# Optimization experiments

Hardware: AMD Instinct MI355X
Metric: run time of the kernel (lower is better)

The kernel has to match this reference:

```python
import jax, jax.numpy as jnp
import numpy as np

H = 64
VOCAB = 64
THRESH_SCALE = 0.4
LN_EPS = 1e-5
NORM_EPS = 1e-12


def setup_inputs() -> dict:
    key = jax.random.key(0)
    ks = jax.random.split(key, 16)
    B, L = 64, 1024
    s = 1.0 / np.sqrt(H)
    inp = {
        "seq": jax.random.randint(ks[0], (B, L), 0, VOCAB),
        "embed_W": jax.random.normal(ks[1], (VOCAB, H), jnp.float32),
        "ff_W1": jax.random.normal(ks[2], (H, 2 * H), jnp.float32) * s,
        "ff_b1": jnp.zeros((2 * H,), jnp.float32),
        "ff_W2": jax.random.normal(ks[3], (2 * H, H), jnp.float32) * s,
        "ff_b2": jnp.zeros((H,), jnp.float32),
        "ln_g": jnp.ones((H,), jnp.float32),
        "ln_b": jnp.zeros((H,), jnp.float32),
        "kp_W": jax.random.normal(ks[4], (H, H), jnp.float32) * s,
        "vp_W": jax.random.normal(ks[5], (H, H), jnp.float32) * s,
        "qp_W": jax.random.normal(ks[6], (H, H), jnp.float32) * s,
        "rp_W": jax.random.normal(ks[7], (H, H), jnp.float32) * s,
        "rp_b": jnp.zeros((H,), jnp.float32),
        "out_W": jax.random.normal(ks[8], (H, VOCAB), jnp.float32) * s,
        "out_b": jnp.zeros((VOCAB,), jnp.float32),
    }
    return inp


def _forward(seq, embed_W, ff_W1, ff_b1, ff_W2, ff_b2, ln_g, ln_b,
             kp_W, vp_W, qp_W, rp_W, rp_b, out_W, out_b):
    h = embed_W[seq]                                    # [B, L, H]
    ff = jnp.maximum(h @ ff_W1 + ff_b1, 0.0) @ ff_W2 + ff_b2
    x = h + ff
    mu = x.mean(-1, keepdims=True)
    var = ((x - mu) ** 2).mean(-1, keepdims=True)       # biased var (torch LayerNorm)
    hn = (x - mu) / jnp.sqrt(var + LN_EPS) * ln_g + ln_b
    B, L, _ = hn.shape

    # Precompute all per-step keys/values, then scan the fast-weight update.
    k_all = hn[:, :-1] @ kp_W                           # [B, L-1, H]
    v_all = hn[:, :-1] @ vp_W                           # [B, L-1, H]
    kn_all = k_all / jnp.maximum(
        jnp.linalg.norm(k_all, axis=-1, keepdims=True), NORM_EPS)

    def step(M, kv):
        kn, v = kv                                      # each [B, H]
        vp = jnp.einsum('bij,bj->bi', M, kn)            # read M along k
        err = jnp.linalg.norm(v - vp, axis=-1)          # [B]
        gate = jnp.where(err > THRESH_SCALE * jnp.linalg.norm(v, axis=-1),
                         1.0, 0.0)                      # hard energy gate
        M = M + gate[:, None, None] * jnp.einsum('bi,bj->bij', v - vp, kn)
        return M, None

    M0 = jnp.zeros((B, H, H), dtype=hn.dtype)
    M, _ = jax.lax.scan(step, M0,
                        (kn_all.transpose(1, 0, 2), v_all.transpose(1, 0, 2)))

    q = hn[:, -1] @ qp_W                                # [B, H]
    r = jnp.einsum('bij,bj->bi', M, q) @ rp_W + rp_b
    return r @ out_W + out_b                            # [B, VOCAB]


def reference(seq, embed_W, ff_W1, ff_b1, ff_W2, ff_b2, ln_g, ln_b,
              kp_W, vp_W, qp_W, rp_W, rp_b, out_W, out_b):
    return _forward(seq, embed_W, ff_W1, ff_b1, ff_W2, ff_b2, ln_g, ln_b,
                    kp_W, vp_W, qp_W, rp_W, rp_b, out_W, out_b)
```

## Files before the change

kernel.cpp:

```cpp
#include <hip/hip_runtime.h>
#include <hip/hip_bf16.h>
#include <math.h>

#define BB 64
#define LL 1024
#define HH 64

typedef float v4f __attribute__((ext_vector_type(4)));
#define F4 __builtin_elementwise_fma

__global__ __launch_bounds__(256, 1)
void token_kernel(const int* __restrict__ seq,
                  const float* __restrict__ embed_W,
                  const float* __restrict__ ff_W1, const float* __restrict__ ff_b1,
                  const float* __restrict__ ff_W2, const float* __restrict__ ff_b2,
                  const float* __restrict__ ln_g, const float* __restrict__ ln_b,
                  const float* __restrict__ kp_W, const float* __restrict__ vp_W,
                  const float* __restrict__ qp_W,
                  float* __restrict__ knv, float* __restrict__ vthr,
                  float* __restrict__ qbuf)
{
    __shared__ __align__(16) float h_s[32][64];
    __shared__ __align__(16) float t1_s[32][128];
    __shared__ __align__(16) float hn_s[32][64];

    const int tid  = threadIdx.x;
    const int tok0 = blockIdx.x * 32;

#pragma unroll
    for (int k = 0; k < 8; ++k) {
        int e   = k * 256 + tid;
        int tok = e >> 6, i = e & 63;
        int s   = seq[tok0 + tok];
        h_s[tok][i] = embed_W[s * 64 + i];
    }
    __syncthreads();

    {
        const int j = tid & 127;
        const int g = tid >> 7;
        float w1c[64];
#pragma unroll
        for (int ii = 0; ii < 64; ++ii) w1c[ii] = ff_W1[ii * 128 + j];
        const float b1j = ff_b1[j];
#pragma unroll
        for (int tk = 0; tk < 16; ++tk) {
            const int tok = g * 16 + tk;
            const float4* h4 = (const float4*)h_s[tok];
            float a0 = b1j, a1 = 0.f, a2 = 0.f, a3 = 0.f;
#pragma unroll
            for (int w = 0; w < 16; ++w) {
                float4 hv = h4[w];
                a0 = fmaf(hv.x, w1c[4*w+0], a0);
                a1 = fmaf(hv.y, w1c[4*w+1], a1);
                a2 = fmaf(hv.z, w1c[4*w+2], a2);
                a3 = fmaf(hv.w, w1c[4*w+3], a3);
            }
            t1_s[tok][j] = fmaxf((a0 + a1) + (a2 + a3), 0.f);
        }
    }
    __syncthreads();

    {
        const int i  = tid & 63;
        const int w4 = tid >> 6;
        const float b2i = ff_b2[i];
        const float gi  = ln_g[i];
        const float bi  = ln_b[i];
        float accf[8];
#pragma unroll
        for (int tk = 0; tk < 8; ++tk) accf[tk] = b2i;
#pragma unroll
        for (int h = 0; h < 2; ++h) {
            float w2c[64];
#pragma unroll
            for (int jj = 0; jj < 64; ++jj) w2c[jj] = ff_W2[(h*64 + jj) * 64 + i];
#pragma unroll
            for (int tk = 0; tk < 8; ++tk) {
                const int tok = w4 * 8 + tk;
                const float4* t4 = (const float4*)&t1_s[tok][h*64];
                float a0 = 0.f, a1 = 0.f, a2 = 0.f, a3 = 0.f;
#pragma unroll
                for (int w = 0; w < 16; ++w) {
                    float4 tv = t4[w];
                    a0 = fmaf(tv.x, w2c[4*w+0], a0);
                    a1 = fmaf(tv.y, w2c[4*w+1], a1);
                    a2 = fmaf(tv.z, w2c[4*w+2], a2);
                    a3 = fmaf(tv.w, w2c[4*w+3], a3);
                }
                accf[tk] += (a0 + a1) + (a2 + a3);
            }
        }
#pragma unroll
        for (int tk = 0; tk < 8; ++tk) {
            const int tok = w4 * 8 + tk;
            float x = h_s[tok][i] + accf[tk];
            float s = x;
#pragma unroll
            for (int m = 32; m > 0; m >>= 1) s += __shfl_xor(s, m);
            float mu = s * (1.f / 64.f);
            float d  = x - mu;
            float s2 = d * d;
#pragma unroll
            for (int m = 32; m > 0; m >>= 1) s2 += __shfl_xor(s2, m);
            float var = s2 * (1.f / 64.f);
            hn_s[tok][i] = d / sqrtf(var + 1e-5f) * gi + bi;
        }
    }
    __syncthreads();

    {
        const int i  = tid & 63;
        const int w4 = tid >> 6;
        float kc[64], vc[64];
#pragma unroll
        for (int ii = 0; ii < 64; ++ii) {
            kc[ii] = kp_W[ii * 64 + i];
            vc[ii] = vp_W[ii * 64 + i];
        }
#pragma unroll
        for (int tk = 0; tk < 8; ++tk) {
            const int tok = w4 * 8 + tk;
            const int tg  = tok0 + tok;
            const int b   = tg >> 10;
            const int t   = tg & 1023;
            const float4* hn4 = (const float4*)hn_s[tok];
            if (t < 1023) {
                float ka0=0.f,ka1=0.f,ka2=0.f,ka3=0.f;
                float va0=0.f,va1=0.f,va2=0.f,va3=0.f;
#pragma unroll
                for (int w = 0; w < 16; ++w) {
                    float4 hv = hn4[w];
                    ka0 = fmaf(hv.x, kc[4*w+0], ka0);
                    ka1 = fmaf(hv.y, kc[4*w+1], ka1);
                    ka2 = fmaf(hv.z, kc[4*w+2], ka2);
                    ka3 = fmaf(hv.w, kc[4*w+3], ka3);
                    va0 = fmaf(hv.x, vc[4*w+0], va0);
                    va1 = fmaf(hv.y, vc[4*w+1], va1);
                    va2 = fmaf(hv.z, vc[4*w+2], va2);
                    va3 = fmaf(hv.w, vc[4*w+3], va3);
                }
                float ka = (ka0 + ka1) + (ka2 + ka3);
                float va = (va0 + va1) + (va2 + va3);
                float kn2 = ka * ka, vn2 = va * va;
#pragma unroll
                for (int m = 32; m > 0; m >>= 1) {
                    kn2 += __shfl_xor(kn2, m);
                    vn2 += __shfl_xor(vn2, m);
                }
                float knorm = fmaxf(sqrtf(kn2), 1e-12f);
                size_t row = ((size_t)b * 1024 + t) * 128;
                knv[row + i]      = ka / knorm;
                knv[row + 64 + i] = va;
                if (i == 0) vthr[b * 1024 + t] = 0.16f * vn2;
            } else {
                float qa0=0.f,qa1=0.f,qa2=0.f,qa3=0.f;
#pragma unroll
                for (int w = 0; w < 16; ++w) {
                    float4 hv = hn4[w];
                    qa0 = fmaf(hv.x, qp_W[(4*w+0)*64 + i], qa0);
                    qa1 = fmaf(hv.y, qp_W[(4*w+1)*64 + i], qa1);
                    qa2 = fmaf(hv.z, qp_W[(4*w+2)*64 + i], qa2);
                    qa3 = fmaf(hv.w, qp_W[(4*w+3)*64 + i], qa3);
                }
                qbuf[b * 64 + i] = (qa0 + qa1) + (qa2 + qa3);
            }
        }
    }
}


template<int CTRL>
__device__ __forceinline__ float dppadd(float x) {
    int y = __builtin_amdgcn_update_dpp(0, __float_as_int(x), CTRL, 0xF, 0xF, true);
    return x + __int_as_float(y);
}

__device__ __forceinline__ float bcast63(float x) {
    return __int_as_float(__builtin_amdgcn_readlane(__float_as_int(x), 63));
}

__device__ __forceinline__ float wave_sum64(float x) {
    x = dppadd<0x111>(x); x = dppadd<0x112>(x);
    x = dppadd<0x114>(x); x = dppadd<0x118>(x);
    x = dppadd<0x142>(x); x = dppadd<0x143>(x);
    return bcast63(x);
}

__device__ __forceinline__ void wsum4(float& a, float& b, float& c, float& d) {
    a = dppadd<0x111>(a); b = dppadd<0x111>(b); c = dppadd<0x111>(c); d = dppadd<0x111>(d);
    a = dppadd<0x112>(a); b = dppadd<0x112>(b); c = dppadd<0x112>(c); d = dppadd<0x112>(d);
    a = dppadd<0x114>(a); b = dppadd<0x114>(b); c = dppadd<0x114>(c); d = dppadd<0x114>(d);
    a = dppadd<0x118>(a); b = dppadd<0x118>(b); c = dppadd<0x118>(c); d = dppadd<0x118>(d);
    a = dppadd<0x142>(a); b = dppadd<0x142>(b); c = dppadd<0x142>(c); d = dppadd<0x142>(d);
    a = dppadd<0x143>(a); b = dppadd<0x143>(b); c = dppadd<0x143>(c); d = dppadd<0x143>(d);
    a = bcast63(a); b = bcast63(b); c = bcast63(c); d = bcast63(d);
}

#define LOADK8(P, ROW) do { \
    const float* rA_ = (ROW) + (wid << 3); \
    const float* rB_ = rA_ + 4; \
    P##A0 = *(const v4f*)(rA_ +  0); P##A1 = *(const v4f*)(rA_ + 16); \
    P##A2 = *(const v4f*)(rA_ + 32); P##A3 = *(const v4f*)(rA_ + 48); \
    P##B0 = *(const v4f*)(rB_ +  0); P##B1 = *(const v4f*)(rB_ + 16); \
    P##B2 = *(const v4f*)(rB_ + 32); P##B3 = *(const v4f*)(rB_ + 48); \
} while (0)

#define UPD8(P, G) do { \
    v4f gv_ = {G, G, G, G}; \
    mA0 = F4(gv_, P##A0, mA0); mA1 = F4(gv_, P##A1, mA1); \
    mA2 = F4(gv_, P##A2, mA2); mA3 = F4(gv_, P##A3, mA3); \
    mB0 = F4(gv_, P##B0, mB0); mB1 = F4(gv_, P##B1, mB1); \
    mB2 = F4(gv_, P##B2, mB2); mB3 = F4(gv_, P##B3, mB3); \
} while (0)

#define CHUNK2(UP, UQ, XR, XS, ROW2, ROW3, TH2P, TH3P, PAR) do { \
    UPD8(UP, gdp); \
    UPD8(UQ, gdq); \
    v4f qa_ = F4(mA0, XR##A0, F4(mA1, XR##A1, F4(mA2, XR##A2, mA3 * XR##A3))); \
    v4f qb_ = F4(mB0, XR##B0, F4(mB1, XR##B1, F4(mB2, XR##B2, mB3 * XR##B3))); \
    v4f q0_ = qa_ + qb_; \
    float own0_ = (q0_.x + q0_.y) + (q0_.z + q0_.w); \
    v4f ra_ = F4(mA0, XS##A0, F4(mA1, XS##A1, F4(mA2, XS##A2, mA3 * XS##A3))); \
    v4f rb_ = F4(mB0, XS##B0, F4(mB1, XS##B1, F4(mB2, XS##B2, mB3 * XS##B3))); \
    v4f r0_ = ra_ + rb_; \
    float own1_ = (r0_.x + r0_.y) + (r0_.z + r0_.w); \
    ((float2*)pex[PAR][wid])[lane] = make_float2(own0_, own1_); \
    asm volatile("s_waitcnt lgkmcnt(0)\n\ts_barrier" ::: "memory"); \
    float2 oth_ = ((const float2*)pex[PAR][1 - wid])[lane]; \
    float knl2_ = (ROW2)[lane]; \
    float knl3_ = (ROW3)[lane]; \
    float vv2_  = (ROW2)[64 + lane]; \
    float vv3_  = (ROW3)[64 + lane]; \
    float th2_  = *(TH2P); \
    float th3_  = *(TH3P); \
    LOADK8(UP, ROW2); \
    LOADK8(UQ, ROW3); \
    float base0_ = own0_ + oth_.x; \
    float base1_ = own1_ + oth_.y; \
    float d00_ = vv0 - base0_; \
    float d01_ = vv1 - base1_; \
    float x0_ = d00_ * d00_, x1_ = d00_ * d01_; \
    float x2_ = d01_ * d01_, x3_ = knl2_ * knl3_; \
    wsum4(x0_, x1_, x2_, x3_); \
    bool g0_ = x0_ > th0; \
    float corr_ = fmaf(2.f * c3, x1_, -(c3 * c3) * x0_); \
    float e1_ = g0_ ? (x2_ - corr_) : x2_; \
    bool g1_ = e1_ > th1; \
    float gd0_ = g0_ ? d00_ : 0.f; \
    float d1_  = fmaf(-c3, gd0_, d01_); \
    gdp = gd0_; \
    gdq = g1_ ? d1_ : 0.f; \
    vv0 = vv2_; vv1 = vv3_; th0 = th2_; th1 = th3_; c3 = x3_; \
} while (0)

#define BUF8(CB, NB, TP) \
    CHUNK2(U,V,S,T,(CB)+2*128, (CB)+3*128, (TP)+2, (TP)+3, 0); \
    CHUNK2(S,T,U,V,(CB)+4*128, (CB)+5*128, (TP)+4, (TP)+5, 1); \
    CHUNK2(U,V,S,T,(CB)+6*128, (CB)+7*128, (TP)+6, (TP)+7, 0); \
    CHUNK2(S,T,U,V,(CB)+8*128, (CB)+9*128, (TP)+8, (TP)+9, 1); \
    CHUNK2(U,V,S,T,(CB)+10*128,(CB)+11*128,(TP)+10,(TP)+11,0); \
    CHUNK2(S,T,U,V,(CB)+12*128,(CB)+13*128,(TP)+12,(TP)+13,1); \
    CHUNK2(U,V,S,T,(CB)+14*128,(CB)+15*128,(TP)+14,(TP)+15,0); \
    CHUNK2(S,T,U,V,(NB)+0*128, (NB)+1*128, (TP)+16,(TP)+17,1);

__device__ __forceinline__ void gl2lds_1k(const float* g, float* l, int lane) {
    __builtin_amdgcn_global_load_lds(
        (const __attribute__((address_space(1))) void*)(g + lane * 4),
        (__attribute__((address_space(3))) void*)l, 16, 0, 0);
}

__device__ __forceinline__ void prefetch_half(const float* g, float* l,
                                              int lane, int wid) {
#pragma unroll
    for (int j = 0; j < 4; ++j)
        gl2lds_1k(g + wid * 1024 + j * 256, l + wid * 1024 + j * 256, lane);
}

__global__ __launch_bounds__(128, 1)
void scan_kernel(const float* __restrict__ knv,
                 const float* __restrict__ vthr,
                 const float* __restrict__ qbuf,
                 const float* __restrict__ rp_W, const float* __restrict__ rp_b,
                 const float* __restrict__ out_W, const float* __restrict__ out_b,
                 float* __restrict__ out)
{
    const int b    = blockIdx.x;
    const int tid  = threadIdx.x;
    const int lane = tid & 63;
    const int wid  = tid >> 6;
    const float* knvb = knv  + (size_t)b * 1024 * 128;
    const float* thrb = vthr + (size_t)b * 1024;

    __shared__ __align__(16) float thr_s[1040];
    __shared__ __align__(16) float buf[3 * 2048];
    __shared__ __align__(16) float pex[2][2][128];
    __shared__ float sh[64];

    v4f mA0={0,0,0,0},mA1={0,0,0,0},mA2={0,0,0,0},mA3={0,0,0,0};
    v4f mB0={0,0,0,0},mB1={0,0,0,0},mB2={0,0,0,0},mB3={0,0,0,0};
    v4f SA0,SA1,SA2,SA3,SB0,SB1,SB2,SB3;
    v4f TA0,TA1,TA2,TA3,TB0,TB1,TB2,TB3;
    v4f UA0,UA1,UA2,UA3,UB0,UB1,UB2,UB3;
    v4f VA0,VA1,VA2,VA3,VB0,VB1,VB2,VB3;

    if (wid == 0) {
#pragma unroll
        for (int w = 0; w < 4; ++w) gl2lds_1k(thrb + w * 256, thr_s + w * 256, lane);
    }
    prefetch_half(knvb,        buf,        lane, wid);
    prefetch_half(knvb + 2048, buf + 2048, lane, wid);
    prefetch_half(knvb + 4096, buf + 4096, lane, wid);

    asm volatile("s_waitcnt vmcnt(4) lgkmcnt(0)\n\ts_barrier" ::: "memory");

    LOADK8(S, buf);
    LOADK8(T, buf + 128);
    {
        v4f z_ = {0.f, 0.f, 0.f, 0.f};
        UA0=z_;UA1=z_;UA2=z_;UA3=z_;UB0=z_;UB1=z_;UB2=z_;UB3=z_;
        VA0=z_;VA1=z_;VA2=z_;VA3=z_;VB0=z_;VB1=z_;VB2=z_;VB3=z_;
    }
    float vv0 = buf[64 + lane];
    float vv1 = buf[192 + lane];
    float th0 = thr_s[0];
    float th1 = thr_s[1];
    float c3  = wave_sum64(buf[lane] * buf[128 + lane]);
    float gdp = 0.f, gdq = 0.f;

#pragma unroll 1
    for (int c = 0; c < 62; ++c) {
        asm volatile("s_waitcnt vmcnt(4)" ::: "memory");
        const float* cb = buf + (c % 3) * 2048;
        const float* nb = buf + ((c + 1) % 3) * 2048;
        const float* tp = thr_s + c * 16;
        BUF8(cb, nb, tp)
        if (c <= 60)
            prefetch_half(knvb + (size_t)(c + 3) * 2048,
                          buf + (c % 3) * 2048, lane, wid);
    }
    asm volatile("s_waitcnt vmcnt(0)" ::: "memory");
    asm volatile("s_barrier" ::: "memory");
    {
        const float* cb = buf + 2 * 2048;
        const float* nb = buf;
        const float* tp = thr_s + 62 * 16;
        BUF8(cb, nb, tp)
    }
    {
        const float* cb = buf;
        const float* nb = buf + 2048;
        const float* tp = thr_s + 63 * 16;
        BUF8(cb, nb, tp)
    }
    UPD8(U, gdp);

    {
        const v4f* qq = (const v4f*)(qbuf + b * 64);
        const int w2 = 2 * wid;
        v4f aqA = F4(mA0, qq[w2+0], F4(mA1, qq[w2+4],
                  F4(mA2, qq[w2+8],  mA3 * qq[w2+12])));
        v4f aqB = F4(mB0, qq[w2+1], F4(mB1, qq[w2+5],
                  F4(mB2, qq[w2+9],  mB3 * qq[w2+13])));
        v4f aq = aqA + aqB;
        float vq_own = (aq.x + aq.y) + (aq.z + aq.w);
        ((float*)pex)[wid * 64 + lane] = vq_own;
        asm volatile("s_waitcnt lgkmcnt(0)\n\ts_barrier" ::: "memory");
        float vq = vq_own + ((float*)pex)[(1 - wid) * 64 + lane];

        if (wid == 0) {
            sh[lane] = vq;
            asm volatile("s_waitcnt lgkmcnt(0)" ::: "memory");
            float r = rp_b[lane];
#pragma unroll
            for (int ii = 0; ii < 64; ++ii) r = fmaf(sh[ii], rp_W[ii * 64 + lane], r);
            asm volatile("s_waitcnt lgkmcnt(0)" ::: "memory");
            sh[lane] = r;
            asm volatile("s_waitcnt lgkmcnt(0)" ::: "memory");
            float o = out_b[lane];
#pragma unroll
            for (int ii = 0; ii < 64; ++ii) o = fmaf(sh[ii], out_W[ii * 64 + lane], o);
            out[b * 64 + lane] = o;
        }
    }
}

extern "C" void kernel_launch(void* const* d_in, const int* in_sizes, int n_in,
                              void* d_out, int out_size, void* d_ws, size_t ws_size,
                              hipStream_t stream)
{
    const int*   seq   = (const int*)  d_in[0];
    const float* embed = (const float*)d_in[1];
    const float* ffW1  = (const float*)d_in[2];
    const float* ffb1  = (const float*)d_in[3];
    const float* ffW2  = (const float*)d_in[4];
    const float* ffb2  = (const float*)d_in[5];
    const float* lng   = (const float*)d_in[6];
    const float* lnb   = (const float*)d_in[7];
    const float* kpW   = (const float*)d_in[8];
    const float* vpW   = (const float*)d_in[9];
    const float* qpW   = (const float*)d_in[10];
    const float* rpW   = (const float*)d_in[11];
    const float* rpb   = (const float*)d_in[12];
    const float* outW  = (const float*)d_in[13];
    const float* outb  = (const float*)d_in[14];
    float* out = (float*)d_out;

    float* knv  = (float*)d_ws;
    float* vthr = knv  + (size_t)64 * 1024 * 128;
    float* qbuf = vthr + (size_t)64 * 1024;

    token_kernel<<<2048, 256, 0, stream>>>(seq, embed, ffW1, ffb1, ffW2, ffb2,
                                           lng, lnb, kpW, vpW, qpW,
                                           knv, vthr, qbuf);
    scan_kernel<<<64, 128, 0, stream>>>(knv, vthr, qbuf,
                                        rpW, rpb, outW, outb, out);
}
```

Measured before the change: 368.6 us.

## Software-pipeline scan step so cross-wave exchange overlaps next step's matvec

Restructures the sequential fast-weight scan so that each step reads the partner wave's partial result written one step earlier, uses a lagged M·k computed before the previous rank-1 updates, and corrects it algebraically with kn dot products (cg0..cg3). This moves the LDS exchange and barrier off the critical dependency chain and batches eight wave reductions together. The prefetch ring grows from three to four buffers so the previous chunk's rows stay resident. It adds extra dot-product reductions and epilogue logic, and its correctness depends on careful buffer indexing.

```diff
diff --git a/kernel.cpp b/kernel.cpp
--- a/kernel.cpp
+++ b/kernel.cpp
@@ -187,14 +187,14 @@
     return bcast63(x);
 }
 
-__device__ __forceinline__ void wsum4(float& a, float& b, float& c, float& d) {
-    a = dppadd<0x111>(a); b = dppadd<0x111>(b); c = dppadd<0x111>(c); d = dppadd<0x111>(d);
-    a = dppadd<0x112>(a); b = dppadd<0x112>(b); c = dppadd<0x112>(c); d = dppadd<0x112>(d);
-    a = dppadd<0x114>(a); b = dppadd<0x114>(b); c = dppadd<0x114>(c); d = dppadd<0x114>(d);
-    a = dppadd<0x118>(a); b = dppadd<0x118>(b); c = dppadd<0x118>(c); d = dppadd<0x118>(d);
-    a = dppadd<0x142>(a); b = dppadd<0x142>(b); c = dppadd<0x142>(c); d = dppadd<0x142>(d);
-    a = dppadd<0x143>(a); b = dppadd<0x143>(b); c = dppadd<0x143>(c); d = dppadd<0x143>(d);
-    a = bcast63(a); b = bcast63(b); c = bcast63(c); d = bcast63(d);
+__device__ __forceinline__ void wsum8(float& a, float& b, float& c, float& d,
+                                      float& e, float& f, float& g, float& h) {
+#define LVL(C) a=dppadd<C>(a); b=dppadd<C>(b); c=dppadd<C>(c); d=dppadd<C>(d); \
+               e=dppadd<C>(e); f=dppadd<C>(f); g=dppadd<C>(g); h=dppadd<C>(h);
+    LVL(0x111) LVL(0x112) LVL(0x114) LVL(0x118) LVL(0x142) LVL(0x143)
+#undef LVL
+    a=bcast63(a); b=bcast63(b); c=bcast63(c); d=bcast63(d);
+    e=bcast63(e); f=bcast63(f); g=bcast63(g); h=bcast63(h);
 }
 
 #define LOADK8(P, ROW) do { \
@@ -214,55 +214,62 @@
     mB2 = F4(gv_, P##B2, mB2); mB3 = F4(gv_, P##B3, mB3); \
 } while (0)
 
-#define CHUNK2(UP, UQ, XR, XS, ROW2, ROW3, TH2P, TH3P, PAR) do { \
-    UPD8(UP, gdp); \
-    UPD8(UQ, gdq); \
-    v4f qa_ = F4(mA0, XR##A0, F4(mA1, XR##A1, F4(mA2, XR##A2, mA3 * XR##A3))); \
-    v4f qb_ = F4(mB0, XR##B0, F4(mB1, XR##B1, F4(mB2, XR##B2, mB3 * XR##B3))); \
+#define BODY(U0R, U1R, X0R, X1R, PK0, PK1, T0P, T1P, PAR) do { \
+    float2 oth_ = ((const float2*)pex[PAR][1 - wid])[lane]; \
+    UPD8(U, gdp); \
+    UPD8(V, gdq); \
+    LOADK8(U, U0R); \
+    LOADK8(V, U1R); \
+    float knl2_ = (PK0)[lane]; \
+    float knl3_ = (PK1)[lane]; \
+    float vv2_  = (PK0)[64 + lane]; \
+    float vv3_  = (PK1)[64 + lane]; \
+    float th2_  = *(T0P); \
+    float th3_  = *(T1P); \
+    v4f qa_ = F4(mA0, SA0, F4(mA1, SA1, F4(mA2, SA2, mA3 * SA3))); \
+    v4f qb_ = F4(mB0, SB0, F4(mB1, SB1, F4(mB2, SB2, mB3 * SB3))); \
     v4f q0_ = qa_ + qb_; \
-    float own0_ = (q0_.x + q0_.y) + (q0_.z + q0_.w); \
-    v4f ra_ = F4(mA0, XS##A0, F4(mA1, XS##A1, F4(mA2, XS##A2, mA3 * XS##A3))); \
-    v4f rb_ = F4(mB0, XS##B0, F4(mB1, XS##B1, F4(mB2, XS##B2, mB3 * XS##B3))); \
+    float own0n_ = (q0_.x + q0_.y) + (q0_.z + q0_.w); \
+    v4f ra_ = F4(mA0, TA0, F4(mA1, TA1, F4(mA2, TA2, mA3 * TA3))); \
+    v4f rb_ = F4(mB0, TB0, F4(mB1, TB1, F4(mB2, TB2, mB3 * TB3))); \
     v4f r0_ = ra_ + rb_; \
-    float own1_ = (r0_.x + r0_.y) + (r0_.z + r0_.w); \
-    ((float2*)pex[PAR][wid])[lane] = make_float2(own0_, own1_); \
+    float own1n_ = (r0_.x + r0_.y) + (r0_.z + r0_.w); \
+    ((float2*)pex[(PAR) ^ 1][wid])[lane] = make_float2(own0n_, own1n_); \
+    LOADK8(S, X0R); \
+    LOADK8(T, X1R); \
+    float base_a_ = pown0 + oth_.x; \
+    float base_b_ = pown1 + oth_.y; \
+    float vp_a_ = fmaf(cg0, gdp, fmaf(cg1, gdq, base_a_)); \
+    float vp_b_ = fmaf(cg2, gdp, fmaf(cg3, gdq, base_b_)); \
+    float da_ = vv_a - vp_a_; \
+    float db_ = vv_b - vp_b_; \
+    float x0_ = da_ * da_, x1_ = da_ * db_, x2_ = db_ * db_; \
+    float y0_ = knl0 * knl2_, y1_ = knl1 * knl2_; \
+    float y2_ = knl0 * knl3_, y3_ = knl1 * knl3_, y4_ = knl2_ * knl3_; \
+    wsum8(x0_, x1_, x2_, y0_, y1_, y2_, y3_, y4_); \
+    bool ga_ = x0_ > th_a; \
+    float corr_ = fmaf(2.f * cab, x1_, -(cab * cab) * x0_); \
+    float eb_ = ga_ ? (x2_ - corr_) : x2_; \
+    bool gb_ = eb_ > th_b; \
+    float gda_ = ga_ ? da_ : 0.f; \
+    float gdb_ = gb_ ? fmaf(-cab, gda_, db_) : 0.f; \
+    gdp = gda_; gdq = gdb_; \
+    cg0 = y0_; cg1 = y1_; cg2 = y2_; cg3 = y3_; cab = y4_; \
+    knl0 = knl2_; knl1 = knl3_; \
+    vv_a = vv2_; vv_b = vv3_; th_a = th2_; th_b = th3_; \
+    pown0 = own0n_; pown1 = own1n_; \
     asm volatile("s_waitcnt lgkmcnt(0)\n\ts_barrier" ::: "memory"); \
-    float2 oth_ = ((const float2*)pex[PAR][1 - wid])[lane]; \
-    float knl2_ = (ROW2)[lane]; \
-    float knl3_ = (ROW3)[lane]; \
-    float vv2_  = (ROW2)[64 + lane]; \
-    float vv3_  = (ROW3)[64 + lane]; \
-    float th2_  = *(TH2P); \
-    float th3_  = *(TH3P); \
-    LOADK8(UP, ROW2); \
-    LOADK8(UQ, ROW3); \
-    float base0_ = own0_ + oth_.x; \
-    float base1_ = own1_ + oth_.y; \
-    float d00_ = vv0 - base0_; \
-    float d01_ = vv1 - base1_; \
-    float x0_ = d00_ * d00_, x1_ = d00_ * d01_; \
-    float x2_ = d01_ * d01_, x3_ = knl2_ * knl3_; \
-    wsum4(x0_, x1_, x2_, x3_); \
-    bool g0_ = x0_ > th0; \
-    float corr_ = fmaf(2.f * c3, x1_, -(c3 * c3) * x0_); \
-    float e1_ = g0_ ? (x2_ - corr_) : x2_; \
-    bool g1_ = e1_ > th1; \
-    float gd0_ = g0_ ? d00_ : 0.f; \
-    float d1_  = fmaf(-c3, gd0_, d01_); \
-    gdp = gd0_; \
-    gdq = g1_ ? d1_ : 0.f; \
-    vv0 = vv2_; vv1 = vv3_; th0 = th2_; th1 = th3_; c3 = x3_; \
 } while (0)
 
-#define BUF8(CB, NB, TP) \
-    CHUNK2(U,V,S,T,(CB)+2*128, (CB)+3*128, (TP)+2, (TP)+3, 0); \
-    CHUNK2(S,T,U,V,(CB)+4*128, (CB)+5*128, (TP)+4, (TP)+5, 1); \
-    CHUNK2(U,V,S,T,(CB)+6*128, (CB)+7*128, (TP)+6, (TP)+7, 0); \
-    CHUNK2(S,T,U,V,(CB)+8*128, (CB)+9*128, (TP)+8, (TP)+9, 1); \
-    CHUNK2(U,V,S,T,(CB)+10*128,(CB)+11*128,(TP)+10,(TP)+11,0); \
-    CHUNK2(S,T,U,V,(CB)+12*128,(CB)+13*128,(TP)+12,(TP)+13,1); \
-    CHUNK2(U,V,S,T,(CB)+14*128,(CB)+15*128,(TP)+14,(TP)+15,0); \
-    CHUNK2(S,T,U,V,(NB)+0*128, (NB)+1*128, (TP)+16,(TP)+17,1);
+#define BUF8_L(PB, CB, NB, TP) \
+    BODY((PB)+14*128,(PB)+15*128,(CB)+2*128,(CB)+3*128,(CB)+0*128,(CB)+1*128,(TP)+0,(TP)+1,0); \
+    BODY((CB)+0*128,(CB)+1*128,(CB)+4*128,(CB)+5*128,(CB)+2*128,(CB)+3*128,(TP)+2,(TP)+3,1); \
+    BODY((CB)+2*128,(CB)+3*128,(CB)+6*128,(CB)+7*128,(CB)+4*128,(CB)+5*128,(TP)+4,(TP)+5,0); \
+    BODY((CB)+4*128,(CB)+5*128,(CB)+8*128,(CB)+9*128,(CB)+6*128,(CB)+7*128,(TP)+6,(TP)+7,1); \
+    BODY((CB)+6*128,(CB)+7*128,(CB)+10*128,(CB)+11*128,(CB)+8*128,(CB)+9*128,(TP)+8,(TP)+9,0); \
+    BODY((CB)+8*128,(CB)+9*128,(CB)+12*128,(CB)+13*128,(CB)+10*128,(CB)+11*128,(TP)+10,(TP)+11,1); \
+    BODY((CB)+10*128,(CB)+11*128,(CB)+14*128,(CB)+15*128,(CB)+12*128,(CB)+13*128,(TP)+12,(TP)+13,0); \
+    BODY((CB)+12*128,(CB)+13*128,(NB)+0*128,(NB)+1*128,(CB)+14*128,(CB)+15*128,(TP)+14,(TP)+15,1);
 
 __device__ __forceinline__ void gl2lds_1k(const float* g, float* l, int lane) {
     __builtin_amdgcn_global_load_lds(
@@ -293,7 +300,7 @@
     const float* thrb = vthr + (size_t)b * 1024;
 
     __shared__ __align__(16) float thr_s[1040];
-    __shared__ __align__(16) float buf[3 * 2048];
+    __shared__ __align__(16) float buf[4 * 2048];
     __shared__ __align__(16) float pex[2][2][128];
     __shared__ float sh[64];
 
@@ -312,48 +319,65 @@
     prefetch_half(knvb + 2048, buf + 2048, lane, wid);
     prefetch_half(knvb + 4096, buf + 4096, lane, wid);
 
+    {
+        float4 z4 = make_float4(0.f, 0.f, 0.f, 0.f);
+        ((float4*)pex)[tid] = z4;
+    }
+
     asm volatile("s_waitcnt vmcnt(4) lgkmcnt(0)\n\ts_barrier" ::: "memory");
 
     LOADK8(S, buf);
     LOADK8(T, buf + 128);
-    {
-        v4f z_ = {0.f, 0.f, 0.f, 0.f};
-        UA0=z_;UA1=z_;UA2=z_;UA3=z_;UB0=z_;UB1=z_;UB2=z_;UB3=z_;
-        VA0=z_;VA1=z_;VA2=z_;VA3=z_;VB0=z_;VB1=z_;VB2=z_;VB3=z_;
-    }
-    float vv0 = buf[64 + lane];
-    float vv1 = buf[192 + lane];
-    float th0 = thr_s[0];
-    float th1 = thr_s[1];
-    float c3  = wave_sum64(buf[lane] * buf[128 + lane]);
+    LOADK8(U, buf);
+    LOADK8(V, buf);
     float gdp = 0.f, gdq = 0.f;
+    float cg0 = 0.f, cg1 = 0.f, cg2 = 0.f, cg3 = 0.f, cab = 0.f;
+    float knl0 = 0.f, knl1 = 0.f;
+    float vv_a = 0.f, vv_b = 0.f;
+    float th_a = 1e30f, th_b = 1e30f;
+    float pown0 = 0.f, pown1 = 0.f;
 
 #pragma unroll 1
     for (int c = 0; c < 62; ++c) {
         asm volatile("s_waitcnt vmcnt(4)" ::: "memory");
-        const float* cb = buf + (c % 3) * 2048;
-        const float* nb = buf + ((c + 1) % 3) * 2048;
+        const float* cb = buf + (c & 3) * 2048;
+        const float* nb = buf + ((c + 1) & 3) * 2048;
+        const float* pb = (c == 0) ? cb : buf + ((c - 1) & 3) * 2048;
         const float* tp = thr_s + c * 16;
-        BUF8(cb, nb, tp)
+        BUF8_L(pb, cb, nb, tp)
         if (c <= 60)
             prefetch_half(knvb + (size_t)(c + 3) * 2048,
-                          buf + (c % 3) * 2048, lane, wid);
+                          buf + ((c + 3) & 3) * 2048, lane, wid);
     }
     asm volatile("s_waitcnt vmcnt(0)" ::: "memory");
     asm volatile("s_barrier" ::: "memory");
     {
+        const float* pb = buf + 1 * 2048;
         const float* cb = buf + 2 * 2048;
+        const float* nb = buf + 3 * 2048;
+        const float* tp = thr_s + 62 * 16;
+        BUF8_L(pb, cb, nb, tp)
+    }
+    {
+        const float* pb = buf + 2 * 2048;
+        const float* cb = buf + 3 * 2048;
         const float* nb = buf;
-        const float* tp = thr_s + 62 * 16;
-        BUF8(cb, nb, tp)
-    }
-    {
-        const float* cb = buf;
-        const float* nb = buf + 2048;
         const float* tp = thr_s + 63 * 16;
-        BUF8(cb, nb, tp)
-    }
-    UPD8(U, gdp);
+        BUF8_L(pb, cb, nb, tp)
+    }
+
+    {
+        float2 oth_ = ((const float2*)pex[0][1 - wid])[lane];
+        UPD8(U, gdp);
+        UPD8(V, gdq);
+        float base_a_ = pown0 + oth_.x;
+        float vp_a_ = fmaf(cg0, gdp, fmaf(cg1, gdq, base_a_));
+        float da_ = vv_a - vp_a_;
+        float e_ = wave_sum64(da_ * da_);
+        float gda_ = (e_ > th_a) ? da_ : 0.f;
+        LOADK8(S, buf + 3 * 2048 + 14 * 128);
+        UPD8(S, gda_);
+    }
 
     {
         const v4f* qq = (const v4f*)(qbuf + b * 64);
```

New measurement: 427.9 us. +16.1%, slower.

## Split scan kernel fast-weight columns across four waves instead of two

Applied to the files above, without the earlier changes.

The sequential scan kernel now uses 256 threads (4 waves) per batch, with each wave holding 16 columns of the 64x64 fast-weight matrix instead of 32. Per-step FMA work and register footprint per wave are halved, and partial dot products are exchanged through LDS among four waves. The trade-off is a 4-wave barrier every two steps and more LDS reads per exchange on what is a latency-bound serial chain. Prefetch is split across four waves accordingly.

```diff
diff --git a/kernel.cpp b/kernel.cpp
--- a/kernel.cpp
+++ b/kernel.cpp
@@ -197,47 +197,41 @@
     a = bcast63(a); b = bcast63(b); c = bcast63(c); d = bcast63(d);
 }
 
-#define LOADK8(P, ROW) do { \
-    const float* rA_ = (ROW) + (wid << 3); \
-    const float* rB_ = rA_ + 4; \
-    P##A0 = *(const v4f*)(rA_ +  0); P##A1 = *(const v4f*)(rA_ + 16); \
-    P##A2 = *(const v4f*)(rA_ + 32); P##A3 = *(const v4f*)(rA_ + 48); \
-    P##B0 = *(const v4f*)(rB_ +  0); P##B1 = *(const v4f*)(rB_ + 16); \
-    P##B2 = *(const v4f*)(rB_ + 32); P##B3 = *(const v4f*)(rB_ + 48); \
+#define LOADK4(P, ROW) do { \
+    const float* r_ = (ROW) + (wid << 4); \
+    P##0 = *(const v4f*)(r_ + 0);  P##1 = *(const v4f*)(r_ + 4); \
+    P##2 = *(const v4f*)(r_ + 8);  P##3 = *(const v4f*)(r_ + 12); \
 } while (0)
 
-#define UPD8(P, G) do { \
+#define UPD4(P, G) do { \
     v4f gv_ = {G, G, G, G}; \
-    mA0 = F4(gv_, P##A0, mA0); mA1 = F4(gv_, P##A1, mA1); \
-    mA2 = F4(gv_, P##A2, mA2); mA3 = F4(gv_, P##A3, mA3); \
-    mB0 = F4(gv_, P##B0, mB0); mB1 = F4(gv_, P##B1, mB1); \
-    mB2 = F4(gv_, P##B2, mB2); mB3 = F4(gv_, P##B3, mB3); \
+    m0 = F4(gv_, P##0, m0); m1 = F4(gv_, P##1, m1); \
+    m2 = F4(gv_, P##2, m2); m3 = F4(gv_, P##3, m3); \
 } while (0)
 
 #define CHUNK2(UP, UQ, XR, XS, ROW2, ROW3, TH2P, TH3P, PAR) do { \
-    UPD8(UP, gdp); \
-    UPD8(UQ, gdq); \
-    v4f qa_ = F4(mA0, XR##A0, F4(mA1, XR##A1, F4(mA2, XR##A2, mA3 * XR##A3))); \
-    v4f qb_ = F4(mB0, XR##B0, F4(mB1, XR##B1, F4(mB2, XR##B2, mB3 * XR##B3))); \
-    v4f q0_ = qa_ + qb_; \
-    float own0_ = (q0_.x + q0_.y) + (q0_.z + q0_.w); \
-    v4f ra_ = F4(mA0, XS##A0, F4(mA1, XS##A1, F4(mA2, XS##A2, mA3 * XS##A3))); \
-    v4f rb_ = F4(mB0, XS##B0, F4(mB1, XS##B1, F4(mB2, XS##B2, mB3 * XS##B3))); \
-    v4f r0_ = ra_ + rb_; \
-    float own1_ = (r0_.x + r0_.y) + (r0_.z + r0_.w); \
+    UPD4(UP, gdp); \
+    UPD4(UQ, gdq); \
+    v4f q_ = F4(m0, XR##0, F4(m1, XR##1, F4(m2, XR##2, m3 * XR##3))); \
+    float own0_ = (q_.x + q_.y) + (q_.z + q_.w); \
+    v4f r_ = F4(m0, XS##0, F4(m1, XS##1, F4(m2, XS##2, m3 * XS##3))); \
+    float own1_ = (r_.x + r_.y) + (r_.z + r_.w); \
     ((float2*)pex[PAR][wid])[lane] = make_float2(own0_, own1_); \
     asm volatile("s_waitcnt lgkmcnt(0)\n\ts_barrier" ::: "memory"); \
-    float2 oth_ = ((const float2*)pex[PAR][1 - wid])[lane]; \
+    float2 p0_ = ((const float2*)pex[PAR][0])[lane]; \
+    float2 p1_ = ((const float2*)pex[PAR][1])[lane]; \
+    float2 p2_ = ((const float2*)pex[PAR][2])[lane]; \
+    float2 p3_ = ((const float2*)pex[PAR][3])[lane]; \
     float knl2_ = (ROW2)[lane]; \
     float knl3_ = (ROW3)[lane]; \
     float vv2_  = (ROW2)[64 + lane]; \
     float vv3_  = (ROW3)[64 + lane]; \
     float th2_  = *(TH2P); \
     float th3_  = *(TH3P); \
-    LOADK8(UP, ROW2); \
-    LOADK8(UQ, ROW3); \
-    float base0_ = own0_ + oth_.x; \
-    float base1_ = own1_ + oth_.y; \
+    LOADK4(UP, ROW2); \
+    LOADK4(UQ, ROW3); \
+    float base0_ = (p0_.x + p1_.x) + (p2_.x + p3_.x); \
+    float base1_ = (p0_.y + p1_.y) + (p2_.y + p3_.y); \
     float d00_ = vv0 - base0_; \
     float d01_ = vv1 - base1_; \
     float x0_ = d00_ * d00_, x1_ = d00_ * d01_; \
@@ -270,14 +264,14 @@
         (__attribute__((address_space(3))) void*)l, 16, 0, 0);
 }
 
-__device__ __forceinline__ void prefetch_half(const float* g, float* l,
-                                              int lane, int wid) {
-#pragma unroll
-    for (int j = 0; j < 4; ++j)
-        gl2lds_1k(g + wid * 1024 + j * 256, l + wid * 1024 + j * 256, lane);
-}
-
-__global__ __launch_bounds__(128, 1)
+__device__ __forceinline__ void prefetch_quarter(const float* g, float* l,
+                                                 int lane, int wid) {
+#pragma unroll
+    for (int j = 0; j < 2; ++j)
+        gl2lds_1k(g + wid * 512 + j * 256, l + wid * 512 + j * 256, lane);
+}
+
+__global__ __launch_bounds__(256, 1)
 void scan_kernel(const float* __restrict__ knv,
                  const float* __restrict__ vthr,
                  const float* __restrict__ qbuf,
@@ -294,32 +288,36 @@
 
     __shared__ __align__(16) float thr_s[1040];
     __shared__ __align__(16) float buf[3 * 2048];
-    __shared__ __align__(16) float pex[2][2][128];
+    __shared__ __align__(16) float pex[2][4][128];
     __shared__ float sh[64];
 
-    v4f mA0={0,0,0,0},mA1={0,0,0,0},mA2={0,0,0,0},mA3={0,0,0,0};
-    v4f mB0={0,0,0,0},mB1={0,0,0,0},mB2={0,0,0,0},mB3={0,0,0,0};
-    v4f SA0,SA1,SA2,SA3,SB0,SB1,SB2,SB3;
-    v4f TA0,TA1,TA2,TA3,TB0,TB1,TB2,TB3;
-    v4f UA0,UA1,UA2,UA3,UB0,UB1,UB2,UB3;
-    v4f VA0,VA1,VA2,VA3,VB0,VB1,VB2,VB3;
+    v4f m0={0,0,0,0}, m1={0,0,0,0}, m2={0,0,0,0}, m3={0,0,0,0};
+    v4f S0,S1,S2,S3;
+    v4f T0,T1,T2,T3;
+    v4f U0,U1,U2,U3;
+    v4f V0,V1,V2,V3;
 
     if (wid == 0) {
 #pragma unroll
         for (int w = 0; w < 4; ++w) gl2lds_1k(thrb + w * 256, thr_s + w * 256, lane);
     }
-    prefetch_half(knvb,        buf,        lane, wid);
-    prefetch_half(knvb + 2048, buf + 2048, lane, wid);
-    prefetch_half(knvb + 4096, buf + 4096, lane, wid);
-
-    asm volatile("s_waitcnt vmcnt(4) lgkmcnt(0)\n\ts_barrier" ::: "memory");
-
-    LOADK8(S, buf);
-    LOADK8(T, buf + 128);
+    prefetch_quarter(knvb,        buf,        lane, wid);
+    prefetch_quarter(knvb + 2048, buf + 2048, lane, wid);
+    prefetch_quarter(knvb + 4096, buf + 4096, lane, wid);
+
+    {
+        float4 z4 = make_float4(0.f, 0.f, 0.f, 0.f);
+        ((float4*)pex)[tid] = z4;
+    }
+
+    asm volatile("s_waitcnt vmcnt(2) lgkmcnt(0)\n\ts_barrier" ::: "memory");
+
+    LOADK4(S, buf);
+    LOADK4(T, buf + 128);
     {
         v4f z_ = {0.f, 0.f, 0.f, 0.f};
-        UA0=z_;UA1=z_;UA2=z_;UA3=z_;UB0=z_;UB1=z_;UB2=z_;UB3=z_;
-        VA0=z_;VA1=z_;VA2=z_;VA3=z_;VB0=z_;VB1=z_;VB2=z_;VB3=z_;
+        U0=z_;U1=z_;U2=z_;U3=z_;
+        V0=z_;V1=z_;V2=z_;V3=z_;
     }
     float vv0 = buf[64 + lane];
     float vv1 = buf[192 + lane];
@@ -330,14 +328,14 @@
 
 #pragma unroll 1
     for (int c = 0; c < 62; ++c) {
-        asm volatile("s_waitcnt vmcnt(4)" ::: "memory");
+        asm volatile("s_waitcnt vmcnt(2)" ::: "memory");
         const float* cb = buf + (c % 3) * 2048;
         const float* nb = buf + ((c + 1) % 3) * 2048;
         const float* tp = thr_s + c * 16;
         BUF8(cb, nb, tp)
         if (c <= 60)
-            prefetch_half(knvb + (size_t)(c + 3) * 2048,
-                          buf + (c % 3) * 2048, lane, wid);
+            prefetch_quarter(knvb + (size_t)(c + 3) * 2048,
+                             buf + (c % 3) * 2048, lane, wid);
     }
     asm volatile("s_waitcnt vmcnt(0)" ::: "memory");
     asm volatile("s_barrier" ::: "memory");
@@ -353,22 +351,20 @@
         const float* tp = thr_s + 63 * 16;
         BUF8(cb, nb, tp)
     }
-    UPD8(U, gdp);
+    UPD4(U, gdp);
 
     {
         const v4f* qq = (const v4f*)(qbuf + b * 64);
-        const int w2 = 2 * wid;
-        v4f aqA = F4(mA0, qq[w2+0], F4(mA1, qq[w2+4],
-                  F4(mA2, qq[w2+8],  mA3 * qq[w2+12])));
-        v4f aqB = F4(mB0, qq[w2+1], F4(mB1, qq[w2+5],
-                  F4(mB2, qq[w2+9],  mB3 * qq[w2+13])));
-        v4f aq = aqA + aqB;
+        const int w4i = 4 * wid;
+        v4f aq = F4(m0, qq[w4i+0], F4(m1, qq[w4i+1],
+                 F4(m2, qq[w4i+2],  m3 * qq[w4i+3])));
         float vq_own = (aq.x + aq.y) + (aq.z + aq.w);
-        ((float*)pex)[wid * 64 + lane] = vq_own;
+        pex[0][wid][lane] = vq_own;
         asm volatile("s_waitcnt lgkmcnt(0)\n\ts_barrier" ::: "memory");
-        float vq = vq_own + ((float*)pex)[(1 - wid) * 64 + lane];
 
         if (wid == 0) {
+            float vq = (pex[0][0][lane] + pex[0][1][lane])
+                     + (pex[0][2][lane] + pex[0][3][lane]);
             sh[lane] = vq;
             asm volatile("s_waitcnt lgkmcnt(0)" ::: "memory");
             float r = rp_b[lane];
@@ -413,6 +409,6 @@
     token_kernel<<<2048, 256, 0, stream>>>(seq, embed, ffW1, ffb1, ffW2, ffb2,
                                            lng, lnb, kpW, vpW, qpW,
                                            knv, vthr, qbuf);
-    scan_kernel<<<64, 128, 0, stream>>>(knv, vthr, qbuf,
+    scan_kernel<<<64, 256, 0, stream>>>(knv, vthr, qbuf,
                                         rpW, rpb, outW, outb, out);
 }
```

New measurement: 366.1 us (median of 2 runs). No clear change (-0.7%).
